# Kernel tuning notes

Measured on AMD Instinct MI355X. Metric: run time of the kernel, lower is better.

The kernel has to match this reference:

```python
import jax, jax.numpy as jnp
import numpy as np

N_NODES = 100000
N_EDGES = 1600000
IN_F, HID, N_CLS = 64, 128, 64


def setup_inputs() -> dict:
    key = jax.random.key(0)
    ks = jax.random.split(key, 7)
    return {
        "x": jax.random.normal(ks[0], (N_NODES, IN_F), dtype=jnp.float32),
        "W1": jax.random.normal(ks[1], (IN_F, HID), dtype=jnp.float32) * (1.0 / np.sqrt(IN_F)),
        "b1": jax.random.normal(ks[2], (HID,), dtype=jnp.float32) * 0.01,
        "W2": jax.random.normal(ks[3], (HID, N_CLS), dtype=jnp.float32) * (1.0 / np.sqrt(HID)),
        "b2": jax.random.normal(ks[4], (N_CLS,), dtype=jnp.float32) * 0.01,
        "src": jax.random.randint(ks[5], (N_EDGES,), 0, N_NODES, dtype=jnp.int32),
        "dst": jax.random.randint(ks[6], (N_EDGES,), 0, N_NODES, dtype=jnp.int32),
    }


def _gcn_layer(x, src, dst, W, b, n_nodes):
    # gather src features per edge, sum-scatter into dst nodes (SpMM), then linear
    agg = jax.ops.segment_sum(x[src], dst, num_segments=n_nodes)  # [N, d]
    return agg @ W + b


def reference(x, W1, b1, W2, b2, src, dst):
    n = x.shape[0]
    h = jax.nn.relu(_gcn_layer(x, src, dst, W1, b1, n))
    return _gcn_layer(h, src, dst, W2, b2, n)
```

## Files before the change

kernel.cpp:

```cpp
#include <hip/hip_runtime.h>

#define N_NODES 100000
#define N_EDGES 1600000
#define IN_F 64
#define HID 128
#define N_CLS 64

#define NPB2 256
#define NBK2 ((N_NODES + NPB2 - 1) / NPB2)
#define NPBLK 512
#define PCHUNK (N_EDGES / NPBLK)
#define CVTBLK ((N_NODES * 64 / 8 + 255) / 256)

__device__ __forceinline__ unsigned short f2bf(float f) {
    unsigned int u = __float_as_uint(f);
    u = (u + 0x7FFFu + ((u >> 16) & 1u)) >> 16;
    return (unsigned short)u;
}
__device__ __forceinline__ float bf2f(unsigned short h) {
    return __uint_as_float(((unsigned int)h) << 16);
}

__global__ void k_zero_f4(float4* __restrict__ p, int n4) {
    int i = blockIdx.x * blockDim.x + threadIdx.x;
    if (i < n4) p[i] = make_float4(0.f, 0.f, 0.f, 0.f);
}
__global__ void k_init_bias(float* __restrict__ out, const float* __restrict__ b2, int n) {
    int i = blockIdx.x * blockDim.x + threadIdx.x;
    if (i < n) out[i] = b2[i & 63];
}

__global__ __launch_bounds__(256) void k_cvt_count(const float4* __restrict__ x4,
                                                   uint4* __restrict__ xh,
                                                   const int* __restrict__ dst,
                                                   int* __restrict__ C) {
    __shared__ int h[NBK2];
    const int t = threadIdx.x;
    if (blockIdx.x < NPBLK) {
        for (int i = t; i < NBK2; i += 256) h[i] = 0;
        __syncthreads();
        const int e0 = blockIdx.x * PCHUNK;
        int e1 = e0 + PCHUNK; if (e1 > N_EDGES) e1 = N_EDGES;
        for (int e = e0 + t; e < e1; e += 256) atomicAdd(&h[dst[e] >> 8], 1);
        __syncthreads();
        for (int i = t; i < NBK2; i += 256) C[blockIdx.x * NBK2 + i] = h[i];
    } else {
        int i = (blockIdx.x - NPBLK) * 256 + t;
        const int n8 = N_NODES * 64 / 8;
        if (i < n8) {
            float4 a = x4[2 * i], b = x4[2 * i + 1];
            uint4 o;
            o.x = (unsigned)f2bf(a.x) | ((unsigned)f2bf(a.y) << 16);
            o.y = (unsigned)f2bf(a.z) | ((unsigned)f2bf(a.w) << 16);
            o.z = (unsigned)f2bf(b.x) | ((unsigned)f2bf(b.y) << 16);
            o.w = (unsigned)f2bf(b.z) | ((unsigned)f2bf(b.w) << 16);
            xh[i] = o;
        }
    }
}

__global__ __launch_bounds__(NPBLK) void k_colscan(int* __restrict__ C,
                                                   int* __restrict__ btot) {
    __shared__ int sc[2][NPBLK];
    const int t = threadIdx.x;
    const int bucket = blockIdx.x;
    int v = C[t * NBK2 + bucket];
    sc[0][t] = v;
    __syncthreads();
    int cur = 0;
    for (int d = 1; d < NPBLK; d <<= 1) {
        int x = sc[cur][t];
        if (t >= d) x += sc[cur][t - d];
        sc[cur ^ 1][t] = x;
        __syncthreads();
        cur ^= 1;
    }
    C[t * NBK2 + bucket] = sc[cur][t] - v;
    if (t == NPBLK - 1) btot[bucket] = sc[cur][t];
}

__global__ __launch_bounds__(512) void k_btscan(const int* __restrict__ btot,
                                                int* __restrict__ boff) {
    __shared__ int sc[2][512];
    const int t = threadIdx.x;
    int v = (t < NBK2) ? btot[t] : 0;
    sc[0][t] = v;
    __syncthreads();
    int cur = 0;
    for (int d = 1; d < 512; d <<= 1) {
        int x = sc[cur][t];
        if (t >= d) x += sc[cur][t - d];
        sc[cur ^ 1][t] = x;
        __syncthreads();
        cur ^= 1;
    }
    if (t < NBK2) boff[t] = sc[cur][t] - v;
    if (t == 0) boff[NBK2] = N_EDGES;
}

__global__ __launch_bounds__(256) void k_scat(const int* __restrict__ src,
                                              const int* __restrict__ dst,
                                              const int* __restrict__ C,
                                              const int* __restrict__ boff,
                                              int* __restrict__ eb) {
    __shared__ int gbase[NBK2];
    __shared__ int lcur[NBK2];
    const int t = threadIdx.x;
    for (int i = t; i < NBK2; i += 256) {
        gbase[i] = boff[i] + C[blockIdx.x * NBK2 + i];
        lcur[i] = 0;
    }
    __syncthreads();
    const int e0 = blockIdx.x * PCHUNK;
    int e1 = e0 + PCHUNK; if (e1 > N_EDGES) e1 = N_EDGES;
    for (int e = e0 + t; e < e1; e += 256) {
        int d = dst[e];
        int b = d >> 8;
        int r = atomicAdd(&lcur[b], 1);
        eb[gbase[b] + r] = ((d & 255) << 17) | src[e];
    }
}

__global__ __launch_bounds__(256) void k_fill3(const int* __restrict__ eb,
                                               const int* __restrict__ boff,
                                               int* __restrict__ off,
                                               int* __restrict__ es) {
    __shared__ int ldeg[NPB2];
    __shared__ int sc[2][NPB2];
    const int t = threadIdx.x;
    const int b = blockIdx.x;
    const int bbase = boff[b], bend = boff[b + 1];

    ldeg[t] = 0;
    __syncthreads();
    for (int i = bbase + t; i < bend; i += 256) atomicAdd(&ldeg[eb[i] >> 17], 1);
    __syncthreads();

    int v = ldeg[t];
    sc[0][t] = v;
    __syncthreads();
    int cur = 0;
    for (int d = 1; d < NPB2; d <<= 1) {
        int x = sc[cur][t];
        if (t >= d) x += sc[cur][t - d];
        sc[cur ^ 1][t] = x;
        __syncthreads();
        cur ^= 1;
    }
    int ex = sc[cur][t] - v;

    const int n0 = b * NPB2;
    if (n0 + t < N_NODES) off[n0 + t] = bbase + ex;
    if (b == NBK2 - 1 && t == 0) off[N_NODES] = N_EDGES;

    ldeg[t] = ex;
    __syncthreads();

    for (int i = bbase + t; i < bend; i += 256) {
        int p = eb[i];
        int r = atomicAdd(&ldeg[p >> 17], 1);
        es[bbase + r] = p & 0x1FFFF;
    }
}

__global__ __launch_bounds__(256) void k_gather4(const uint2* __restrict__ feat,
                                                 const int* __restrict__ es,
                                                 const int* __restrict__ off,
                                                 const float* __restrict__ bias,
                                                 float* __restrict__ out) {
    const int wave = threadIdx.x >> 6;
    const int lane = threadIdx.x & 63;
    const int grp = lane >> 4;
    const int l16 = lane & 15;
    const int n = blockIdx.x * 16 + wave * 4 + grp;
    const int beg = off[n], end = off[n + 1];
    const int gb = grp << 4;
    float a0 = 0.f, a1 = 0.f, a2 = 0.f, a3 = 0.f;
    for (int base = beg; base < end; base += 16) {
        int m = end - base; if (m > 16) m = 16;
        int id = (l16 < m) ? es[base + l16] : 0;
        int k = 0;
        for (; k + 4 <= m; k += 4) {
            int s0 = __shfl(id, gb | (k + 0));
            int s1 = __shfl(id, gb | (k + 1));
            int s2 = __shfl(id, gb | (k + 2));
            int s3 = __shfl(id, gb | (k + 3));
            uint2 u0 = feat[(unsigned)s0 * 16u + l16];
            uint2 u1 = feat[(unsigned)s1 * 16u + l16];
            uint2 u2 = feat[(unsigned)s2 * 16u + l16];
            uint2 u3 = feat[(unsigned)s3 * 16u + l16];
            a0 += (__uint_as_float(u0.x << 16) + __uint_as_float(u1.x << 16))
                + (__uint_as_float(u2.x << 16) + __uint_as_float(u3.x << 16));
            a1 += (__uint_as_float(u0.x & 0xFFFF0000u) + __uint_as_float(u1.x & 0xFFFF0000u))
                + (__uint_as_float(u2.x & 0xFFFF0000u) + __uint_as_float(u3.x & 0xFFFF0000u));
            a2 += (__uint_as_float(u0.y << 16) + __uint_as_float(u1.y << 16))
                + (__uint_as_float(u2.y << 16) + __uint_as_float(u3.y << 16));
            a3 += (__uint_as_float(u0.y & 0xFFFF0000u) + __uint_as_float(u1.y & 0xFFFF0000u))
                + (__uint_as_float(u2.y & 0xFFFF0000u) + __uint_as_float(u3.y & 0xFFFF0000u));
        }
        for (; k < m; ++k) {
            int s = __shfl(id, gb | k);
            uint2 u = feat[(unsigned)s * 16u + l16];
            a0 += __uint_as_float(u.x << 16);
            a1 += __uint_as_float(u.x & 0xFFFF0000u);
            a2 += __uint_as_float(u.y << 16);
            a3 += __uint_as_float(u.y & 0xFFFF0000u);
        }
    }
    if (bias) {
        float4 bv = *(const float4*)&bias[l16 * 4];
        a0 += bv.x; a1 += bv.y; a2 += bv.z; a3 += bv.w;
    }
    float4 o; o.x = a0; o.y = a1; o.z = a2; o.w = a3;
    *(float4*)&out[(size_t)n * 64 + l16 * 4] = o;
}

__global__ void k_scatter64(const float* __restrict__ feat,
                            const int* __restrict__ src,
                            const int* __restrict__ dst,
                            float* __restrict__ out) {
    int i = blockIdx.x * blockDim.x + threadIdx.x;
    int e = i >> 4;
    if (e >= N_EDGES) return;
    int j = (i & 15) << 2;
    int s = src[e];
    int d = dst[e];
    float4 v = *reinterpret_cast<const float4*>(feat + (size_t)s * 64 + j);
    float* o = out + (size_t)d * 64 + j;
    atomicAdd(o + 0, v.x);
    atomicAdd(o + 1, v.y);
    atomicAdd(o + 2, v.z);
    atomicAdd(o + 3, v.w);
}

#define MROWS 32
#define XS_S 68
#define HS2_S 152

__device__ __forceinline__ void fma4(float4& a, float s, const float4& wv) {
    a.x = fmaf(s, wv.x, a.x);
    a.y = fmaf(s, wv.y, a.y);
    a.z = fmaf(s, wv.z, a.z);
    a.w = fmaf(s, wv.w, a.w);
}

__global__ __launch_bounds__(256, 3) void k_gemm1(const float* __restrict__ A,
                                                  unsigned short* __restrict__ H,
                                                  const float* __restrict__ W1,
                                                  const float* __restrict__ b1) {
    __shared__ float Ws[64 * 128];
    __shared__ float xs[MROWS * XS_S];
    __shared__ float b1s[128];
    const int t = threadIdx.x;
    const int row0 = blockIdx.x * MROWS;

    {
        const float4* w4 = (const float4*)W1;
        float4* s4 = (float4*)Ws;
        for (int i = t; i < 2048; i += 256) s4[i] = w4[i];
    }
    if (t < 128) b1s[t] = b1[t];
#pragma unroll
    for (int c = 0; c < 2; ++c) {
        int lin = t + c * 256;
        int r = lin >> 4, k4 = lin & 15;
        float4 v = *(const float4*)(A + (size_t)(row0 + r) * 64 + k4 * 4);
        *(float4*)&xs[r * XS_S + k4 * 4] = v;
    }
    __syncthreads();

    const int rg = t >> 5, cg = t & 31;
    const int r0 = rg * 4, c0 = cg * 4;
    float4 bv = *(const float4*)&b1s[c0];
    float4 acc0 = bv, acc1 = bv, acc2 = bv, acc3 = bv;
#pragma unroll 4
    for (int k4 = 0; k4 < 16; ++k4) {
        float4 a0 = *(const float4*)&xs[(r0 + 0) * XS_S + k4 * 4];
        float4 a1 = *(const float4*)&xs[(r0 + 1) * XS_S + k4 * 4];
        float4 a2 = *(const float4*)&xs[(r0 + 2) * XS_S + k4 * 4];
        float4 a3 = *(const float4*)&xs[(r0 + 3) * XS_S + k4 * 4];
        float4 w0 = *(const float4*)&Ws[(k4 * 4 + 0) * 128 + c0];
        float4 w1 = *(const float4*)&Ws[(k4 * 4 + 1) * 128 + c0];
        float4 w2 = *(const float4*)&Ws[(k4 * 4 + 2) * 128 + c0];
        float4 w3 = *(const float4*)&Ws[(k4 * 4 + 3) * 128 + c0];
        fma4(acc0, a0.x, w0); fma4(acc0, a0.y, w1); fma4(acc0, a0.z, w2); fma4(acc0, a0.w, w3);
        fma4(acc1, a1.x, w0); fma4(acc1, a1.y, w1); fma4(acc1, a1.z, w2); fma4(acc1, a1.w, w3);
        fma4(acc2, a2.x, w0); fma4(acc2, a2.y, w1); fma4(acc2, a2.z, w2); fma4(acc2, a2.w, w3);
        fma4(acc3, a3.x, w0); fma4(acc3, a3.y, w1); fma4(acc3, a3.z, w2); fma4(acc3, a3.w, w3);
    }
    ushort4 o;
    o.x = f2bf(fmaxf(acc0.x, 0.f)); o.y = f2bf(fmaxf(acc0.y, 0.f));
    o.z = f2bf(fmaxf(acc0.z, 0.f)); o.w = f2bf(fmaxf(acc0.w, 0.f));
    *(ushort4*)&H[(size_t)(row0 + r0 + 0) * 128 + c0] = o;
    o.x = f2bf(fmaxf(acc1.x, 0.f)); o.y = f2bf(fmaxf(acc1.y, 0.f));
    o.z = f2bf(fmaxf(acc1.z, 0.f)); o.w = f2bf(fmaxf(acc1.w, 0.f));
    *(ushort4*)&H[(size_t)(row0 + r0 + 1) * 128 + c0] = o;
    o.x = f2bf(fmaxf(acc2.x, 0.f)); o.y = f2bf(fmaxf(acc2.y, 0.f));
    o.z = f2bf(fmaxf(acc2.z, 0.f)); o.w = f2bf(fmaxf(acc2.w, 0.f));
    *(ushort4*)&H[(size_t)(row0 + r0 + 2) * 128 + c0] = o;
    o.x = f2bf(fmaxf(acc3.x, 0.f)); o.y = f2bf(fmaxf(acc3.y, 0.f));
    o.z = f2bf(fmaxf(acc3.z, 0.f)); o.w = f2bf(fmaxf(acc3.w, 0.f));
    *(ushort4*)&H[(size_t)(row0 + r0 + 3) * 128 + c0] = o;
}

__global__ __launch_bounds__(256, 3) void k_gemm2(const unsigned short* __restrict__ H,
                                                  unsigned short* __restrict__ zh,
                                                  const float* __restrict__ W2) {
    __shared__ float Ws[128 * 64];
    __shared__ unsigned short hsb[MROWS * HS2_S];
    const int t = threadIdx.x;
    const int row0 = blockIdx.x * MROWS;

    {
        const float4* w4 = (const float4*)W2;
        float4* s4 = (float4*)Ws;
        for (int i = t; i < 2048; i += 256) s4[i] = w4[i];
    }
#pragma unroll
    for (int c = 0; c < 2; ++c) {
        int lin = t + c * 256;
        int r = lin >> 4, k8 = lin & 15;
        uint4 v = *(const uint4*)(H + (size_t)(row0 + r) * 128 + k8 * 8);
        *(uint4*)&hsb[r * HS2_S + k8 * 8] = v;
    }
    __syncthreads();

    const int rg = t >> 4, cg = t & 15;
    const int r0 = rg * 2, c0 = cg * 4;
    float4 acc0 = make_float4(0.f, 0.f, 0.f, 0.f);
    float4 acc1 = make_float4(0.f, 0.f, 0.f, 0.f);
#pragma unroll 4
    for (int k4 = 0; k4 < 32; ++k4) {
        ushort4 u0 = *(const ushort4*)&hsb[(r0 + 0) * HS2_S + k4 * 4];
        ushort4 u1 = *(const ushort4*)&hsb[(r0 + 1) * HS2_S + k4 * 4];
        float4 w0 = *(const float4*)&Ws[(k4 * 4 + 0) * 64 + c0];
        float4 w1 = *(const float4*)&Ws[(k4 * 4 + 1) * 64 + c0];
        float4 w2 = *(const float4*)&Ws[(k4 * 4 + 2) * 64 + c0];
        float4 w3 = *(const float4*)&Ws[(k4 * 4 + 3) * 64 + c0];
        fma4(acc0, bf2f(u0.x), w0); fma4(acc0, bf2f(u0.y), w1);
        fma4(acc0, bf2f(u0.z), w2); fma4(acc0, bf2f(u0.w), w3);
        fma4(acc1, bf2f(u1.x), w0); fma4(acc1, bf2f(u1.y), w1);
        fma4(acc1, bf2f(u1.z), w2); fma4(acc1, bf2f(u1.w), w3);
    }
    ushort4 o0, o1;
    o0.x = f2bf(acc0.x); o0.y = f2bf(acc0.y); o0.z = f2bf(acc0.z); o0.w = f2bf(acc0.w);
    o1.x = f2bf(acc1.x); o1.y = f2bf(acc1.y); o1.z = f2bf(acc1.z); o1.w = f2bf(acc1.w);
    *(ushort4*)&zh[(size_t)(row0 + r0 + 0) * 64 + c0] = o0;
    *(ushort4*)&zh[(size_t)(row0 + r0 + 1) * 64 + c0] = o1;
}

__global__ __launch_bounds__(256, 2) void k_mlpF(float* __restrict__ A,
                                                 const float* __restrict__ W1,
                                                 const float* __restrict__ b1,
                                                 const float* __restrict__ W2) {
    __shared__ float Ws[64 * 128];
    __shared__ float xs[MROWS * XS_S];
    __shared__ float hs[MROWS * 132];
    __shared__ float b1s[128];
    const int t = threadIdx.x;
    const int row0 = blockIdx.x * MROWS;

    {
        const float4* w4 = (const float4*)W1;
        float4* s4 = (float4*)Ws;
        for (int i = t; i < 2048; i += 256) s4[i] = w4[i];
    }
    if (t < 128) b1s[t] = b1[t];
#pragma unroll
    for (int c = 0; c < 2; ++c) {
        int lin = t + c * 256;
        int r = lin >> 4, k4 = lin & 15;
        float4 v = *(const float4*)(A + (size_t)(row0 + r) * 64 + k4 * 4);
        *(float4*)&xs[r * XS_S + k4 * 4] = v;
    }
    __syncthreads();
    {
        const int rg = t >> 5, cg = t & 31;
        const int r0 = rg * 4, c0 = cg * 4;
        float4 bv = *(const float4*)&b1s[c0];
        float4 acc0 = bv, acc1 = bv, acc2 = bv, acc3 = bv;
#pragma unroll 4
        for (int k4 = 0; k4 < 16; ++k4) {
            float4 a0 = *(const float4*)&xs[(r0 + 0) * XS_S + k4 * 4];
            float4 a1 = *(const float4*)&xs[(r0 + 1) * XS_S + k4 * 4];
            float4 a2 = *(const float4*)&xs[(r0 + 2) * XS_S + k4 * 4];
            float4 a3 = *(const float4*)&xs[(r0 + 3) * XS_S + k4 * 4];
            float4 w0 = *(const float4*)&Ws[(k4 * 4 + 0) * 128 + c0];
            float4 w1 = *(const float4*)&Ws[(k4 * 4 + 1) * 128 + c0];
            float4 w2 = *(const float4*)&Ws[(k4 * 4 + 2) * 128 + c0];
            float4 w3 = *(const float4*)&Ws[(k4 * 4 + 3) * 128 + c0];
            fma4(acc0, a0.x, w0); fma4(acc0, a0.y, w1); fma4(acc0, a0.z, w2); fma4(acc0, a0.w, w3);
            fma4(acc1, a1.x, w0); fma4(acc1, a1.y, w1); fma4(acc1, a1.z, w2); fma4(acc1, a1.w, w3);
            fma4(acc2, a2.x, w0); fma4(acc2, a2.y, w1); fma4(acc2, a2.z, w2); fma4(acc2, a2.w, w3);
            fma4(acc3, a3.x, w0); fma4(acc3, a3.y, w1); fma4(acc3, a3.z, w2); fma4(acc3, a3.w, w3);
        }
        float4 h;
        h.x = fmaxf(acc0.x, 0.f); h.y = fmaxf(acc0.y, 0.f); h.z = fmaxf(acc0.z, 0.f); h.w = fmaxf(acc0.w, 0.f);
        *(float4*)&hs[(r0 + 0) * 132 + c0] = h;
        h.x = fmaxf(acc1.x, 0.f); h.y = fmaxf(acc1.y, 0.f); h.z = fmaxf(acc1.z, 0.f); h.w = fmaxf(acc1.w, 0.f);
        *(float4*)&hs[(r0 + 1) * 132 + c0] = h;
        h.x = fmaxf(acc2.x, 0.f); h.y = fmaxf(acc2.y, 0.f); h.z = fmaxf(acc2.z, 0.f); h.w = fmaxf(acc2.w, 0.f);
        *(float4*)&hs[(r0 + 2) * 132 + c0] = h;
        h.x = fmaxf(acc3.x, 0.f); h.y = fmaxf(acc3.y, 0.f); h.z = fmaxf(acc3.z, 0.f); h.w = fmaxf(acc3.w, 0.f);
        *(float4*)&hs[(r0 + 3) * 132 + c0] = h;
    }
    __syncthreads();
    {
        const float4* w4 = (const float4*)W2;
        float4* s4 = (float4*)Ws;
        for (int i = t; i < 2048; i += 256) s4[i] = w4[i];
    }
    __syncthreads();
    {
        const int rg = t >> 4, cg = t & 15;
        const int r0 = rg * 2, c0 = cg * 4;
        float4 acc0 = make_float4(0.f, 0.f, 0.f, 0.f);
        float4 acc1 = make_float4(0.f, 0.f, 0.f, 0.f);
#pragma unroll 4
        for (int k4 = 0; k4 < 32; ++k4) {
            float4 h0 = *(const float4*)&hs[(r0 + 0) * 132 + k4 * 4];
            float4 h1 = *(const float4*)&hs[(r0 + 1) * 132 + k4 * 4];
            float4 w0 = *(const float4*)&Ws[(k4 * 4 + 0) * 64 + c0];
            float4 w1 = *(const float4*)&Ws[(k4 * 4 + 1) * 64 + c0];
            float4 w2 = *(const float4*)&Ws[(k4 * 4 + 2) * 64 + c0];
            float4 w3 = *(const float4*)&Ws[(k4 * 4 + 3) * 64 + c0];
            fma4(acc0, h0.x, w0); fma4(acc0, h0.y, w1); fma4(acc0, h0.z, w2); fma4(acc0, h0.w, w3);
            fma4(acc1, h1.x, w0); fma4(acc1, h1.y, w1); fma4(acc1, h1.z, w2); fma4(acc1, h1.w, w3);
        }
        *(float4*)(A + (size_t)(row0 + r0 + 0) * 64 + c0) = acc0;
        *(float4*)(A + (size_t)(row0 + r0 + 1) * 64 + c0) = acc1;
    }
}

static inline size_t alignup(size_t v, size_t a) { return (v + a - 1) & ~(a - 1); }

extern "C" void kernel_launch(void* const* d_in, const int* in_sizes, int n_in,
                              void* d_out, int out_size, void* d_ws, size_t ws_size,
                              hipStream_t stream) {
    const float* x  = (const float*)d_in[0];
    const float* W1 = (const float*)d_in[1];
    const float* b1 = (const float*)d_in[2];
    const float* W2 = (const float*)d_in[3];
    const float* b2 = (const float*)d_in[4];
    const int* src  = (const int*)d_in[5];
    const int* dst  = (const int*)d_in[6];
    float* out = (float*)d_out;

    const int nfeat = N_NODES * 64;
    const int nfeat4 = nfeat / 4;

    char* base = (char*)d_ws;
    size_t o = 0;
    size_t o_xh   = o;   o = alignup(o + (size_t)nfeat * 2, 64);
    size_t o_es   = o;   o = alignup(o + (size_t)N_EDGES * 4, 64);
    size_t o_off  = o;   o = alignup(o + (size_t)(N_NODES + 1) * 4, 64);
    size_t o_C    = o;   o = alignup(o + (size_t)NPBLK * NBK2 * 4, 64);
    size_t o_btot = o;   o = alignup(o + (size_t)NBK2 * 4, 64);
    size_t o_boff = o;   o = alignup(o + (size_t)(NBK2 + 1) * 4, 64);
    size_t o_shrd = o;   o = alignup(o + (size_t)nfeat * 4, 64);
    size_t need1 = o;

    unsigned short* xh = (unsigned short*)(base + o_xh);
    int* es    = (int*)(base + o_es);
    int* off   = (int*)(base + o_off);
    int* C     = (int*)(base + o_C);
    int* btot  = (int*)(base + o_btot);
    int* boff  = (int*)(base + o_boff);
    int* eb    = (int*)(base + o_shrd);
    float* A   = (float*)(base + o_shrd);
    unsigned short* H = (unsigned short*)(base + o_shrd);
    unsigned short* zh = xh;

    if (ws_size >= need1) {
        k_cvt_count<<<NPBLK + CVTBLK, 256, 0, stream>>>((const float4*)x, (uint4*)xh, dst, C);
        k_colscan<<<NBK2, NPBLK, 0, stream>>>(C, btot);
        k_btscan<<<1, 512, 0, stream>>>(btot, boff);
        k_scat<<<NPBLK, 256, 0, stream>>>(src, dst, C, boff, eb);
        k_fill3<<<NBK2, 256, 0, stream>>>(eb, boff, off, es);

        k_gather4<<<N_NODES / 16, 256, 0, stream>>>((const uint2*)xh, es, off, nullptr, A);
        k_gemm1<<<N_NODES / MROWS, 256, 0, stream>>>(A, H, W1, b1);
        k_gemm2<<<N_NODES / MROWS, 256, 0, stream>>>(H, zh, W2);
        k_gather4<<<N_NODES / 16, 256, 0, stream>>>((const uint2*)zh, es, off, b2, out);
    } else {
        float* A3 = (float*)d_ws;
        k_zero_f4<<<(nfeat4 + 255) / 256, 256, 0, stream>>>((float4*)A3, nfeat4);
        int threads = N_EDGES * 16;
        k_scatter64<<<(threads + 255) / 256, 256, 0, stream>>>(x, src, dst, A3);
        k_mlpF<<<N_NODES / MROWS, 256, 0, stream>>>(A3, W1, b1, W2);
        k_init_bias<<<(nfeat + 255) / 256, 256, 0, stream>>>(out, b2, nfeat);
        k_scatter64<<<(threads + 255) / 256, 256, 0, stream>>>(A3, src, dst, out);
    }
}
```

Before: 178.6 us.

## Fold bucket-total scan into scatter kernels and widen gather to 16-byte loads

Removes the separate single-block bucket-offset scan kernel: both k_scat and k_fill3 now recompute the exclusive scan of bucket totals locally, two buckets per thread. This saves one launch and a serial dependency, at the cost of redundant scan work in every block. The gather kernel is also changed from 16 lanes per node with 8-byte bf16 loads to 8 lanes per node with 16-byte loads and 8 accumulators. That halves the lanes per node and doubles the bytes per load instruction.

```diff
diff --git a/kernel.cpp b/kernel.cpp
--- a/kernel.cpp
+++ b/kernel.cpp
@@ -79,36 +79,36 @@
     if (t == NPBLK - 1) btot[bucket] = sc[cur][t];
 }
 
-__global__ __launch_bounds__(512) void k_btscan(const int* __restrict__ btot,
-                                                int* __restrict__ boff) {
-    __shared__ int sc[2][512];
-    const int t = threadIdx.x;
-    int v = (t < NBK2) ? btot[t] : 0;
-    sc[0][t] = v;
+__global__ __launch_bounds__(256) void k_scat(const int* __restrict__ src,
+                                              const int* __restrict__ dst,
+                                              const int* __restrict__ C,
+                                              const int* __restrict__ btot,
+                                              int* __restrict__ eb) {
+    __shared__ int gbase[NBK2];
+    __shared__ int lcur[NBK2];
+    __shared__ int sc[2][256];
+    const int t = threadIdx.x;
+    int v0 = (2 * t < NBK2) ? btot[2 * t] : 0;
+    int v1 = (2 * t + 1 < NBK2) ? btot[2 * t + 1] : 0;
+    int s = v0 + v1;
+    sc[0][t] = s;
     __syncthreads();
     int cur = 0;
-    for (int d = 1; d < 512; d <<= 1) {
+    for (int d = 1; d < 256; d <<= 1) {
         int x = sc[cur][t];
         if (t >= d) x += sc[cur][t - d];
         sc[cur ^ 1][t] = x;
         __syncthreads();
         cur ^= 1;
     }
-    if (t < NBK2) boff[t] = sc[cur][t] - v;
-    if (t == 0) boff[NBK2] = N_EDGES;
-}
-
-__global__ __launch_bounds__(256) void k_scat(const int* __restrict__ src,
-                                              const int* __restrict__ dst,
-                                              const int* __restrict__ C,
-                                              const int* __restrict__ boff,
-                                              int* __restrict__ eb) {
-    __shared__ int gbase[NBK2];
-    __shared__ int lcur[NBK2];
-    const int t = threadIdx.x;
-    for (int i = t; i < NBK2; i += 256) {
-        gbase[i] = boff[i] + C[blockIdx.x * NBK2 + i];
-        lcur[i] = 0;
+    int exp = sc[cur][t] - s;
+    if (2 * t < NBK2) {
+        gbase[2 * t] = exp + C[blockIdx.x * NBK2 + 2 * t];
+        lcur[2 * t] = 0;
+    }
+    if (2 * t + 1 < NBK2) {
+        gbase[2 * t + 1] = exp + v0 + C[blockIdx.x * NBK2 + 2 * t + 1];
+        lcur[2 * t + 1] = 0;
     }
     __syncthreads();
     const int e0 = blockIdx.x * PCHUNK;
@@ -122,14 +122,33 @@
 }
 
 __global__ __launch_bounds__(256) void k_fill3(const int* __restrict__ eb,
-                                               const int* __restrict__ boff,
+                                               const int* __restrict__ btot,
                                                int* __restrict__ off,
                                                int* __restrict__ es) {
     __shared__ int ldeg[NPB2];
     __shared__ int sc[2][NPB2];
+    __shared__ int sh_base, sh_end;
     const int t = threadIdx.x;
     const int b = blockIdx.x;
-    const int bbase = boff[b], bend = boff[b + 1];
+
+    int v0 = (2 * t < NBK2) ? btot[2 * t] : 0;
+    int v1 = (2 * t + 1 < NBK2) ? btot[2 * t + 1] : 0;
+    int s = v0 + v1;
+    sc[0][t] = s;
+    __syncthreads();
+    int cur = 0;
+    for (int d = 1; d < 256; d <<= 1) {
+        int x = sc[cur][t];
+        if (t >= d) x += sc[cur][t - d];
+        sc[cur ^ 1][t] = x;
+        __syncthreads();
+        cur ^= 1;
+    }
+    int exp = sc[cur][t] - s;
+    if (2 * t == b)     { sh_base = exp;          sh_end = exp + v0; }
+    if (2 * t + 1 == b) { sh_base = exp + v0;     sh_end = exp + v0 + v1; }
+    __syncthreads();
+    const int bbase = sh_base, bend = sh_end;
 
     ldeg[t] = 0;
     __syncthreads();
@@ -139,7 +158,7 @@
     int v = ldeg[t];
     sc[0][t] = v;
     __syncthreads();
-    int cur = 0;
+    cur = 0;
     for (int d = 1; d < NPB2; d <<= 1) {
         int x = sc[cur][t];
         if (t >= d) x += sc[cur][t - d];
@@ -163,32 +182,33 @@
     }
 }
 
-__global__ __launch_bounds__(256) void k_gather4(const uint2* __restrict__ feat,
+__global__ __launch_bounds__(256) void k_gather8(const uint4* __restrict__ feat,
                                                  const int* __restrict__ es,
                                                  const int* __restrict__ off,
                                                  const float* __restrict__ bias,
                                                  float* __restrict__ out) {
     const int wave = threadIdx.x >> 6;
     const int lane = threadIdx.x & 63;
-    const int grp = lane >> 4;
-    const int l16 = lane & 15;
-    const int n = blockIdx.x * 16 + wave * 4 + grp;
+    const int grp = lane >> 3;
+    const int l8 = lane & 7;
+    const int n = blockIdx.x * 32 + wave * 8 + grp;
     const int beg = off[n], end = off[n + 1];
-    const int gb = grp << 4;
+    const int gb = grp << 3;
     float a0 = 0.f, a1 = 0.f, a2 = 0.f, a3 = 0.f;
-    for (int base = beg; base < end; base += 16) {
-        int m = end - base; if (m > 16) m = 16;
-        int id = (l16 < m) ? es[base + l16] : 0;
+    float a4 = 0.f, a5 = 0.f, a6 = 0.f, a7 = 0.f;
+    for (int base = beg; base < end; base += 8) {
+        int m = end - base; if (m > 8) m = 8;
+        int id = (l8 < m) ? es[base + l8] : 0;
         int k = 0;
         for (; k + 4 <= m; k += 4) {
             int s0 = __shfl(id, gb | (k + 0));
             int s1 = __shfl(id, gb | (k + 1));
             int s2 = __shfl(id, gb | (k + 2));
             int s3 = __shfl(id, gb | (k + 3));
-            uint2 u0 = feat[(unsigned)s0 * 16u + l16];
-            uint2 u1 = feat[(unsigned)s1 * 16u + l16];
-            uint2 u2 = feat[(unsigned)s2 * 16u + l16];
-            uint2 u3 = feat[(unsigned)s3 * 16u + l16];
+            uint4 u0 = feat[(unsigned)s0 * 8u + l8];
+            uint4 u1 = feat[(unsigned)s1 * 8u + l8];
+            uint4 u2 = feat[(unsigned)s2 * 8u + l8];
+            uint4 u3 = feat[(unsigned)s3 * 8u + l8];
             a0 += (__uint_as_float(u0.x << 16) + __uint_as_float(u1.x << 16))
                 + (__uint_as_float(u2.x << 16) + __uint_as_float(u3.x << 16));
             a1 += (__uint_as_float(u0.x & 0xFFFF0000u) + __uint_as_float(u1.x & 0xFFFF0000u))
@@ -197,22 +217,39 @@
                 + (__uint_as_float(u2.y << 16) + __uint_as_float(u3.y << 16));
             a3 += (__uint_as_float(u0.y & 0xFFFF0000u) + __uint_as_float(u1.y & 0xFFFF0000u))
                 + (__uint_as_float(u2.y & 0xFFFF0000u) + __uint_as_float(u3.y & 0xFFFF0000u));
+            a4 += (__uint_as_float(u0.z << 16) + __uint_as_float(u1.z << 16))
+                + (__uint_as_float(u2.z << 16) + __uint_as_float(u3.z << 16));
+            a5 += (__uint_as_float(u0.z & 0xFFFF0000u) + __uint_as_float(u1.z & 0xFFFF0000u))
+                + (__uint_as_float(u2.z & 0xFFFF0000u) + __uint_as_float(u3.z & 0xFFFF0000u));
+            a6 += (__uint_as_float(u0.w << 16) + __uint_as_float(u1.w << 16))
+                + (__uint_as_float(u2.w << 16) + __uint_as_float(u3.w << 16));
+            a7 += (__uint_as_float(u0.w & 0xFFFF0000u) + __uint_as_float(u1.w & 0xFFFF0000u))
+                + (__uint_as_float(u2.w & 0xFFFF0000u) + __uint_as_float(u3.w & 0xFFFF0000u));
         }
         for (; k < m; ++k) {
             int s = __shfl(id, gb | k);
-            uint2 u = feat[(unsigned)s * 16u + l16];
+            uint4 u = feat[(unsigned)s * 8u + l8];
             a0 += __uint_as_float(u.x << 16);
             a1 += __uint_as_float(u.x & 0xFFFF0000u);
             a2 += __uint_as_float(u.y << 16);
             a3 += __uint_as_float(u.y & 0xFFFF0000u);
+            a4 += __uint_as_float(u.z << 16);
+            a5 += __uint_as_float(u.z & 0xFFFF0000u);
+            a6 += __uint_as_float(u.w << 16);
+            a7 += __uint_as_float(u.w & 0xFFFF0000u);
         }
     }
     if (bias) {
-        float4 bv = *(const float4*)&bias[l16 * 4];
-        a0 += bv.x; a1 += bv.y; a2 += bv.z; a3 += bv.w;
-    }
-    float4 o; o.x = a0; o.y = a1; o.z = a2; o.w = a3;
-    *(float4*)&out[(size_t)n * 64 + l16 * 4] = o;
+        float4 b0 = *(const float4*)&bias[l8 * 8];
+        float4 b1 = *(const float4*)&bias[l8 * 8 + 4];
+        a0 += b0.x; a1 += b0.y; a2 += b0.z; a3 += b0.w;
+        a4 += b1.x; a5 += b1.y; a6 += b1.z; a7 += b1.w;
+    }
+    float4 o0, o1;
+    o0.x = a0; o0.y = a1; o0.z = a2; o0.w = a3;
+    o1.x = a4; o1.y = a5; o1.z = a6; o1.w = a7;
+    *(float4*)&out[(size_t)n * 64 + l8 * 8] = o0;
+    *(float4*)&out[(size_t)n * 64 + l8 * 8 + 4] = o1;
 }
 
 __global__ void k_scatter64(const float* __restrict__ feat,
@@ -456,7 +493,6 @@
     size_t o_off  = o;   o = alignup(o + (size_t)(N_NODES + 1) * 4, 64);
     size_t o_C    = o;   o = alignup(o + (size_t)NPBLK * NBK2 * 4, 64);
     size_t o_btot = o;   o = alignup(o + (size_t)NBK2 * 4, 64);
-    size_t o_boff = o;   o = alignup(o + (size_t)(NBK2 + 1) * 4, 64);
     size_t o_shrd = o;   o = alignup(o + (size_t)nfeat * 4, 64);
     size_t need1 = o;
 
@@ -465,7 +501,6 @@
     int* off   = (int*)(base + o_off);
     int* C     = (int*)(base + o_C);
     int* btot  = (int*)(base + o_btot);
-    int* boff  = (int*)(base + o_boff);
     int* eb    = (int*)(base + o_shrd);
     float* A   = (float*)(base + o_shrd);
     unsigned short* H = (unsigned short*)(base + o_shrd);
@@ -474,14 +509,13 @@
     if (ws_size >= need1) {
         k_cvt_count<<<NPBLK + CVTBLK, 256, 0, stream>>>((const float4*)x, (uint4*)xh, dst, C);
         k_colscan<<<NBK2, NPBLK, 0, stream>>>(C, btot);
-        k_btscan<<<1, 512, 0, stream>>>(btot, boff);
-        k_scat<<<NPBLK, 256, 0, stream>>>(src, dst, C, boff, eb);
-        k_fill3<<<NBK2, 256, 0, stream>>>(eb, boff, off, es);
-
-        k_gather4<<<N_NODES / 16, 256, 0, stream>>>((const uint2*)xh, es, off, nullptr, A);
+        k_scat<<<NPBLK, 256, 0, stream>>>(src, dst, C, btot, eb);
+        k_fill3<<<NBK2, 256, 0, stream>>>(eb, btot, off, es);
+
+        k_gather8<<<N_NODES / 32, 256, 0, stream>>>((const uint4*)xh, es, off, nullptr, A);
         k_gemm1<<<N_NODES / MROWS, 256, 0, stream>>>(A, H, W1, b1);
         k_gemm2<<<N_NODES / MROWS, 256, 0, stream>>>(H, zh, W2);
-        k_gather4<<<N_NODES / 16, 256, 0, stream>>>((const uint2*)zh, es, off, b2, out);
+        k_gather8<<<N_NODES / 32, 256, 0, stream>>>((const uint4*)zh, es, off, b2, out);
     } else {
         float* A3 = (float*)d_ws;
         k_zero_f4<<<(nfeat4 + 255) / 256, 256, 0, stream>>>((float4*)A3, nfeat4);
```

New measurement: 177.5 us. About the same (-0.6%).
